# Performance work log

Hardware: AMD Instinct MI355X
Metric: run time of the kernel (lower is better)

The kernel has to match this reference:

```python
import jax, jax.numpy as jnp
import numpy as np

B, T, C = 2, 2048, 1024
H, D = 16, 64
EPS = 1e-6


def _layernorm(x, gamma, beta):
    # Faithful to the torch module: uses unbiased std (Bessel) and divides by (std + eps).
    mean = x.mean(-1, keepdims=True)
    std = jnp.sqrt(jnp.sum((x - mean) ** 2, axis=-1, keepdims=True) / (x.shape[-1] - 1))
    return gamma * (x - mean) / (std + EPS) + beta


def setup_inputs() -> dict:
    key = jax.random.key(0)
    ks = jax.random.split(key, 9)
    s = lambda fan_in: 1.0 / np.sqrt(fan_in)
    return {
        "x": jax.random.normal(ks[0], (B, T, C), dtype=jnp.float32),
        "qkv_w": jax.random.uniform(ks[1], (3 * C, C), jnp.float32, -s(C), s(C)),
        "proj_w": jax.random.uniform(ks[2], (C, C), jnp.float32, -s(C), s(C)),
        "proj_b": jax.random.uniform(ks[3], (C,), jnp.float32, -s(C), s(C)),
        "l1_w": jax.random.uniform(ks[4], (4 * C, C), jnp.float32, -s(C), s(C)),
        "l1_b": jax.random.uniform(ks[5], (4 * C,), jnp.float32, -s(C), s(C)),
        "l3_w": jax.random.uniform(ks[6], (C, 4 * C), jnp.float32, -s(4 * C), s(4 * C)),
        "l3_b": jax.random.uniform(ks[7], (C,), jnp.float32, -s(4 * C), s(4 * C)),
        "ln1_g": jnp.ones((C,), jnp.float32),
        "ln1_b": jnp.zeros((C,), jnp.float32),
        "ln2_g": jnp.ones((C,), jnp.float32),
        "ln2_b": jnp.zeros((C,), jnp.float32),
    }


def _attention(x, qkv_w, proj_w, proj_b):
    Bx, Tx, Cx = x.shape
    qkv = x @ qkv_w.T                      # [B,T,3C]
    q, k, v = jnp.split(qkv, 3, axis=-1)
    q = q.reshape(Bx, Tx, H, D)
    k = k.reshape(Bx, Tx, H, D)
    v = v.reshape(Bx, Tx, H, D)
    scores = jnp.einsum("bthd,bshd->bhts", q, k) * (D ** -0.5)  # [B,H,T,T]
    causal = jnp.tril(jnp.ones((Tx, Tx), dtype=bool))
    scores = jnp.where(causal, scores, -jnp.inf)
    attn = jax.nn.softmax(scores, axis=-1)
    out = jnp.einsum("bhts,bshd->bthd", attn, v).reshape(Bx, Tx, Cx)
    return out @ proj_w.T + proj_b


def _mlp(x, l1_w, l1_b, l3_w, l3_b):
    h = jax.nn.relu(x @ l1_w.T + l1_b)     # [B,T,4C]
    return h @ l3_w.T + l3_b


def reference(x, qkv_w, proj_w, proj_b, l1_w, l1_b, l3_w, l3_b, ln1_g, ln1_b, ln2_g, ln2_b):
    # Dropout is identity in eval mode.
    x1 = x + _attention(_layernorm(x, ln1_g, ln1_b), qkv_w, proj_w, proj_b)
    x2 = x1 + _mlp(_layernorm(x1, ln2_g, ln2_b), l1_w, l1_b, l3_w, l3_b)
    return x2
```

## Files before the change

### kernel.cpp

```cpp
#include <hip/hip_runtime.h>

typedef unsigned short u16;
typedef short short8 __attribute__((ext_vector_type(8)));
typedef float floatx4 __attribute__((ext_vector_type(4)));

#define TT 2048
#define CC 1024

__device__ __forceinline__ u16 f2bf(float f) {
  unsigned int u = __float_as_uint(f);
  u += 0x7fffu + ((u >> 16) & 1u);
  return (u16)(u >> 16);
}

__device__ __forceinline__ void glds16(const u16* g, u16* l) {
  __builtin_amdgcn_global_load_lds((const __attribute__((address_space(1))) void*)g,
                                   (__attribute__((address_space(3))) void*)l, 16, 0, 0);
}

__global__ __launch_bounds__(256) void cvt_all_kernel(const float* __restrict__ w0,
                                                      const float* __restrict__ w1,
                                                      const float* __restrict__ w2,
                                                      const float* __restrict__ w3,
                                                      u16* __restrict__ o0,
                                                      u16* __restrict__ o1,
                                                      u16* __restrict__ o2,
                                                      u16* __restrict__ o3) {
  int blk = blockIdx.x;
  const float* in;
  u16* out;
  int base;
  if (blk < 3072)      { in = w0; out = o0; base = 0; }
  else if (blk < 4096) { in = w1; out = o1; base = 3072; }
  else if (blk < 8192) { in = w2; out = o2; base = 4096; }
  else                 { in = w3; out = o3; base = 8192; }
  int i = (blk - base) * 256 + threadIdx.x;
  float4 v = ((const float4*)in)[i];
  ushort4 o;
  o.x = f2bf(v.x); o.y = f2bf(v.y); o.z = f2bf(v.z); o.w = f2bf(v.w);
  ((ushort4*)out)[i] = o;
}

__global__ __launch_bounds__(256) void ln_kernel(const float* __restrict__ x,
                                                 const float* __restrict__ g,
                                                 const float* __restrict__ b,
                                                 u16* __restrict__ out) {
  int row = blockIdx.x;
  int tid = threadIdx.x;
  const float4* xr = (const float4*)(x + (size_t)row * CC);
  float4 v = xr[tid];
  float s = v.x + v.y + v.z + v.w;
  float sq = v.x * v.x + v.y * v.y + v.z * v.z + v.w * v.w;
#pragma unroll
  for (int off = 1; off < 64; off <<= 1) {
    s += __shfl_xor(s, off);
    sq += __shfl_xor(sq, off);
  }
  __shared__ float ss[4], ssq[4];
  int wave = tid >> 6;
  if ((tid & 63) == 0) { ss[wave] = s; ssq[wave] = sq; }
  __syncthreads();
  s = ss[0] + ss[1] + ss[2] + ss[3];
  sq = ssq[0] + ssq[1] + ssq[2] + ssq[3];
  float mean = s * (1.0f / CC);
  float var = (sq - (float)CC * mean * mean) * (1.0f / (CC - 1));
  float inv = 1.0f / (sqrtf(fmaxf(var, 0.0f)) + 1e-6f);
  float4 gv = ((const float4*)g)[tid];
  float4 bv = ((const float4*)b)[tid];
  ushort4 o;
  o.x = f2bf(gv.x * (v.x - mean) * inv + bv.x);
  o.y = f2bf(gv.y * (v.y - mean) * inv + bv.y);
  o.z = f2bf(gv.z * (v.z - mean) * inv + bv.z);
  o.w = f2bf(gv.w * (v.w - mean) * inv + bv.w);
  ((ushort4*)(out + (size_t)row * CC))[tid] = o;
}

template <int BM, int MODE>
__global__ __launch_bounds__(256) void gemm_bt(const u16* __restrict__ A,
                                               const u16* __restrict__ W,
                                               const float* __restrict__ bias,
                                               const float* __restrict__ resid,
                                               float* __restrict__ outf,
                                               u16* __restrict__ outb,
                                               int M, int N, int K) {
  constexpr int MI = BM / 32;
  __shared__ u16 a_lds[BM * 64];
  __shared__ u16 b_lds[128 * 64];
  int tid = threadIdx.x;
  int w = tid >> 6, lane = tid & 63;
  int l15 = lane & 15, quad = lane >> 4;
  int wm = (w >> 1) * (MI * 16), wn = (w & 1) * 64;
  int tm = blockIdx.x * BM, tn = blockIdx.y * 128;
  floatx4 acc[MI][4];
#pragma unroll
  for (int i = 0; i < MI; i++)
#pragma unroll
    for (int j = 0; j < 4; j++) acc[i][j] = (floatx4){0.f, 0.f, 0.f, 0.f};

  int rsub = lane >> 3;
  int cg = (lane & 7) ^ rsub;
  const u16* Ag = A + (size_t)(tm + w * (BM / 4) + rsub) * K + cg * 8;
  const u16* Bg = W + (size_t)(tn + w * 32 + rsub) * K + cg * 8;
  u16* aL = a_lds + w * (BM / 4) * 64;
  u16* bL = b_lds + w * 32 * 64;

  int x = l15 & 7;
  int offA[MI], offB[4];
#pragma unroll
  for (int i = 0; i < MI; i++) offA[i] = (wm + i * 16 + l15) * 64 + ((quad ^ x) * 8);
#pragma unroll
  for (int j = 0; j < 4; j++) offB[j] = (wn + j * 16 + l15) * 64 + ((quad ^ x) * 8);

  for (int k0 = 0; k0 < K; k0 += 64) {
    __syncthreads();
#pragma unroll
    for (int is = 0; is < BM / 32; is++) glds16(Ag + k0 + is * 8 * K, aL + is * 512);
#pragma unroll
    for (int is = 0; is < 4; is++) glds16(Bg + k0 + is * 8 * K, bL + is * 512);
    __syncthreads();
#pragma unroll
    for (int s = 0; s < 2; s++) {
      short8 af[MI], bw[4];
#pragma unroll
      for (int i = 0; i < MI; i++) af[i] = *(const short8*)(a_lds + (offA[i] ^ (s << 5)));
#pragma unroll
      for (int j = 0; j < 4; j++) bw[j] = *(const short8*)(b_lds + (offB[j] ^ (s << 5)));
#pragma unroll
      for (int i = 0; i < MI; i++)
#pragma unroll
        for (int j = 0; j < 4; j++)
          acc[i][j] = __builtin_amdgcn_mfma_f32_16x16x32_bf16(af[i], bw[j], acc[i][j], 0, 0, 0);
    }
  }

#pragma unroll
  for (int i = 0; i < MI; i++) {
    int row0 = tm + wm + i * 16 + quad * 4;
#pragma unroll
    for (int j = 0; j < 4; j++) {
      int col = tn + wn + j * 16 + l15;
      float bb = (MODE != 0) ? bias[col] : 0.0f;
#pragma unroll
      for (int r = 0; r < 4; r++) {
        int row = row0 + r;
        float v = acc[i][j][r];
        if (MODE == 0) {
          if (col < 1024) v *= 0.125f;
          outb[(size_t)row * N + col] = f2bf(v);
        } else if (MODE == 1) {
          outf[(size_t)row * N + col] = v + bb + resid[(size_t)row * N + col];
        } else {
          outb[(size_t)row * N + col] = f2bf(fmaxf(v + bb, 0.0f));
        }
      }
    }
  }
}

__global__ __launch_bounds__(256) void flash_kernel(const u16* __restrict__ qkv,
                                                    u16* __restrict__ attn) {
  int bid = blockIdx.x;
  int qt = 31 - (bid >> 5);
  int bh = bid & 31;
  int b = bh >> 4, h = bh & 15;
  int tid = threadIdx.x, w = tid >> 6, lane = tid & 63;
  int l15 = lane & 15, quad = lane >> 4;

  __shared__ u16 k_lds[64 * 64];
  __shared__ u16 vt_lds[64 * 72];
  __shared__ u16 p_lds[4][16 * 72];

  int qbase = qt * 64 + w * 16;
  const u16* qp = qkv + (size_t)(b * TT + qbase + l15) * 3072 + h * 64;
  short8 qf0 = *(const short8*)(qp + quad * 8);
  short8 qf1 = *(const short8*)(qp + 32 + quad * 8);

  float m_i = -3.0e38f, l_i = 0.0f;
  floatx4 accO[4];
#pragma unroll
  for (int jf = 0; jf < 4; jf++) accO[jf] = (floatx4){0.f, 0.f, 0.f, 0.f};

  int rsub = lane >> 3;
  int cg = (lane & 7) ^ rsub;
  const u16* Kg = qkv + (size_t)(b * TT + w * 16 + rsub) * 3072 + 1024 + h * 64 + cg * 8;
  u16* kL = k_lds + w * 16 * 64;
  int sV = tid & 63, d0v = (tid >> 6) * 16;
  const u16* Vg = qkv + (size_t)(b * TT + sV) * 3072 + 2048 + h * 64 + d0v;

  int x = l15 & 7;
  int kOff[4], vOff[4];
#pragma unroll
  for (int i = 0; i < 4; i++) kOff[i] = (i * 16 + l15) * 64 + ((quad ^ x) * 8);
#pragma unroll
  for (int jf = 0; jf < 4; jf++) vOff[jf] = (jf * 16 + l15) * 72 + quad * 8;
  int pRd = l15 * 72 + quad * 8;

  int kt_end = qt + 1;
  for (int kt = 0; kt < kt_end; kt++) {
    int s0 = kt * 64;
    size_t soff = (size_t)s0 * 3072;
    uint4 v0 = *(const uint4*)(Vg + soff);
    uint4 v1 = *(const uint4*)(Vg + soff + 8);
    __syncthreads();
#pragma unroll
    for (int is = 0; is < 2; is++) glds16(Kg + soff + (size_t)is * 8 * 3072, kL + is * 512);
    {
      u16 tmp[16];
      *(uint4*)tmp = v0;
      *(uint4*)(tmp + 8) = v1;
#pragma unroll
      for (int j = 0; j < 16; j++) vt_lds[(d0v + j) * 72 + sV] = tmp[j];
    }
    __syncthreads();

    floatx4 st[4];
#pragma unroll
    for (int i = 0; i < 4; i++) st[i] = (floatx4){0.f, 0.f, 0.f, 0.f};
#pragma unroll
    for (int i = 0; i < 4; i++) {
      short8 kf0 = *(const short8*)(k_lds + kOff[i]);
      short8 kf1 = *(const short8*)(k_lds + (kOff[i] ^ 32));
      st[i] = __builtin_amdgcn_mfma_f32_16x16x32_bf16(kf0, qf0, st[i], 0, 0, 0);
      st[i] = __builtin_amdgcn_mfma_f32_16x16x32_bf16(kf1, qf1, st[i], 0, 0, 0);
    }

    if (s0 + 63 > qbase + 15) {
      int mg = qbase + l15;
#pragma unroll
      for (int i = 0; i < 4; i++)
#pragma unroll
        for (int r = 0; r < 4; r++) {
          int s = s0 + i * 16 + quad * 4 + r;
          if (s > mg) st[i][r] = -3.0e38f;
        }
    }

    float mx = st[0][0];
#pragma unroll
    for (int i = 0; i < 4; i++)
#pragma unroll
      for (int r = 0; r < 4; r++) mx = fmaxf(mx, st[i][r]);
    mx = fmaxf(mx, __shfl_xor(mx, 16));
    mx = fmaxf(mx, __shfl_xor(mx, 32));
    float mnew = fmaxf(m_i, mx);
    float alpha = __expf(m_i - mnew);
    float ts = 0.0f;
#pragma unroll
    for (int i = 0; i < 4; i++)
#pragma unroll
      for (int r = 0; r < 4; r++) {
        float p = __expf(st[i][r] - mnew);
        st[i][r] = p;
        ts += p;
      }
    ts += __shfl_xor(ts, 16);
    ts += __shfl_xor(ts, 32);
    l_i = l_i * alpha + ts;
    m_i = mnew;

    float aR[4];
#pragma unroll
    for (int r = 0; r < 4; r++) aR[r] = __shfl(alpha, quad * 4 + r);
#pragma unroll
    for (int jf = 0; jf < 4; jf++)
#pragma unroll
      for (int r = 0; r < 4; r++) accO[jf][r] *= aR[r];

#pragma unroll
    for (int i = 0; i < 4; i++) {
      unsigned int lo = (unsigned int)f2bf(st[i][0]) | ((unsigned int)f2bf(st[i][1]) << 16);
      unsigned int hi = (unsigned int)f2bf(st[i][2]) | ((unsigned int)f2bf(st[i][3]) << 16);
      uint2 pk = {lo, hi};
      *(uint2*)(p_lds[w] + l15 * 72 + i * 16 + quad * 4) = pk;
    }

    short8 pf0 = *(const short8*)(p_lds[w] + pRd);
    short8 pf1 = *(const short8*)(p_lds[w] + pRd + 32);
#pragma unroll
    for (int jf = 0; jf < 4; jf++) {
      short8 vf0 = *(const short8*)(vt_lds + vOff[jf]);
      short8 vf1 = *(const short8*)(vt_lds + vOff[jf] + 32);
      accO[jf] = __builtin_amdgcn_mfma_f32_16x16x32_bf16(pf0, vf0, accO[jf], 0, 0, 0);
      accO[jf] = __builtin_amdgcn_mfma_f32_16x16x32_bf16(pf1, vf1, accO[jf], 0, 0, 0);
    }
  }

  float invl = 1.0f / l_i;
  float iR[4];
#pragma unroll
  for (int r = 0; r < 4; r++) iR[r] = __shfl(invl, quad * 4 + r);
  int orow = b * TT + qbase + quad * 4;
#pragma unroll
  for (int r = 0; r < 4; r++) {
    u16* op = attn + (size_t)(orow + r) * CC + h * 64 + l15;
#pragma unroll
    for (int jf = 0; jf < 4; jf++) op[jf * 16] = f2bf(accO[jf][r] * iR[r]);
  }
}

extern "C" void kernel_launch(void* const* d_in, const int* in_sizes, int n_in,
                              void* d_out, int out_size, void* d_ws, size_t ws_size,
                              hipStream_t stream) {
  const float* x      = (const float*)d_in[0];
  const float* qkv_w  = (const float*)d_in[1];
  const float* proj_w = (const float*)d_in[2];
  const float* proj_b = (const float*)d_in[3];
  const float* l1_w   = (const float*)d_in[4];
  const float* l1_b   = (const float*)d_in[5];
  const float* l3_w   = (const float*)d_in[6];
  const float* l3_b   = (const float*)d_in[7];
  const float* ln1_g  = (const float*)d_in[8];
  const float* ln1_b  = (const float*)d_in[9];
  const float* ln2_g  = (const float*)d_in[10];
  const float* ln2_b  = (const float*)d_in[11];
  float* out = (float*)d_out;
  char* ws = (char*)d_ws;

  u16* w_qkv  = (u16*)(ws + 0);
  u16* w_proj = (u16*)(ws + 6291456);
  u16* w_l1   = (u16*)(ws + 8388608);
  u16* w_l3   = (u16*)(ws + 16777216);
  u16* lnb    = (u16*)(ws + 25165824);
  u16* qkvb   = (u16*)(ws + 33554432);
  u16* attnb  = (u16*)(ws + 58720256);
  float* x1   = (float*)(ws + 67108864);
  u16* hb     = (u16*)(ws + 83886080);

  cvt_all_kernel<<<12288, 256, 0, stream>>>(qkv_w, proj_w, l1_w, l3_w,
                                            w_qkv, w_proj, w_l1, w_l3);

  ln_kernel<<<4096, 256, 0, stream>>>(x, ln1_g, ln1_b, lnb);
  gemm_bt<128, 0><<<dim3(32, 24), 256, 0, stream>>>(lnb, w_qkv, nullptr, nullptr, nullptr,
                                                    qkvb, 4096, 3072, 1024);
  flash_kernel<<<1024, 256, 0, stream>>>(qkvb, attnb);
  gemm_bt<64, 1><<<dim3(64, 8), 256, 0, stream>>>(attnb, w_proj, proj_b, x, x1, nullptr,
                                                  4096, 1024, 1024);
  ln_kernel<<<4096, 256, 0, stream>>>(x1, ln2_g, ln2_b, lnb);
  gemm_bt<128, 2><<<dim3(32, 32), 256, 0, stream>>>(lnb, w_l1, l1_b, nullptr, nullptr, hb,
                                                    4096, 4096, 1024);
  gemm_bt<64, 1><<<dim3(64, 8), 256, 0, stream>>>(hb, w_l3, l3_b, x1, out, nullptr,
                                                  4096, 1024, 4096);
}
```

Baseline: 350.2 us.

## Split-K the final MLP GEMM and widen flash-attention key tiles to 128

The last MLP GEMM (K=4096) is split into two K halves launched along grid z. Each half writes fp32 partials into a reused workspace region, and a separate reduce kernel adds the partials, bias and residual. This doubles the block count for a GEMM that previously had only 512 blocks. Separately, the flash kernel now processes 128 keys per iteration instead of 64, halving loop overhead and barriers at the cost of more LDS and registers. The split-K path adds extra fp32 global traffic.

```diff
diff --git a/kernel.cpp b/kernel.cpp
--- a/kernel.cpp
+++ b/kernel.cpp
@@ -82,7 +82,7 @@
                                                const float* __restrict__ resid,
                                                float* __restrict__ outf,
                                                u16* __restrict__ outb,
-                                               int M, int N, int K) {
+                                               int M, int N, int K, int lda) {
   constexpr int MI = BM / 32;
   __shared__ u16 a_lds[BM * 64];
   __shared__ u16 b_lds[128 * 64];
@@ -91,6 +91,7 @@
   int l15 = lane & 15, quad = lane >> 4;
   int wm = (w >> 1) * (MI * 16), wn = (w & 1) * 64;
   int tm = blockIdx.x * BM, tn = blockIdx.y * 128;
+  size_t koff = (size_t)blockIdx.z * K;
   floatx4 acc[MI][4];
 #pragma unroll
   for (int i = 0; i < MI; i++)
@@ -99,8 +100,8 @@
 
   int rsub = lane >> 3;
   int cg = (lane & 7) ^ rsub;
-  const u16* Ag = A + (size_t)(tm + w * (BM / 4) + rsub) * K + cg * 8;
-  const u16* Bg = W + (size_t)(tn + w * 32 + rsub) * K + cg * 8;
+  const u16* Ag = A + (size_t)(tm + w * (BM / 4) + rsub) * lda + koff + cg * 8;
+  const u16* Bg = W + (size_t)(tn + w * 32 + rsub) * lda + koff + cg * 8;
   u16* aL = a_lds + w * (BM / 4) * 64;
   u16* bL = b_lds + w * 32 * 64;
 
@@ -114,9 +115,9 @@
   for (int k0 = 0; k0 < K; k0 += 64) {
     __syncthreads();
 #pragma unroll
-    for (int is = 0; is < BM / 32; is++) glds16(Ag + k0 + is * 8 * K, aL + is * 512);
-#pragma unroll
-    for (int is = 0; is < 4; is++) glds16(Bg + k0 + is * 8 * K, bL + is * 512);
+    for (int is = 0; is < BM / 32; is++) glds16(Ag + k0 + (size_t)is * 8 * lda, aL + is * 512);
+#pragma unroll
+    for (int is = 0; is < 4; is++) glds16(Bg + k0 + (size_t)is * 8 * lda, bL + is * 512);
     __syncthreads();
 #pragma unroll
     for (int s = 0; s < 2; s++) {
@@ -133,13 +134,14 @@
     }
   }
 
+  float* po = (MODE == 3) ? outf + (size_t)blockIdx.z * M * N : outf;
 #pragma unroll
   for (int i = 0; i < MI; i++) {
     int row0 = tm + wm + i * 16 + quad * 4;
 #pragma unroll
     for (int j = 0; j < 4; j++) {
       int col = tn + wn + j * 16 + l15;
-      float bb = (MODE != 0) ? bias[col] : 0.0f;
+      float bb = (MODE == 1 || MODE == 2) ? bias[col] : 0.0f;
 #pragma unroll
       for (int r = 0; r < 4; r++) {
         int row = row0 + r;
@@ -149,12 +151,31 @@
           outb[(size_t)row * N + col] = f2bf(v);
         } else if (MODE == 1) {
           outf[(size_t)row * N + col] = v + bb + resid[(size_t)row * N + col];
+        } else if (MODE == 2) {
+          outb[(size_t)row * N + col] = f2bf(fmaxf(v + bb, 0.0f));
         } else {
-          outb[(size_t)row * N + col] = f2bf(fmaxf(v + bb, 0.0f));
+          po[(size_t)row * N + col] = v;
         }
       }
     }
   }
+}
+
+__global__ __launch_bounds__(256) void reduce2_kernel(const float* __restrict__ p,
+                                                      const float* __restrict__ bias,
+                                                      const float* __restrict__ resid,
+                                                      float* __restrict__ out) {
+  int i = blockIdx.x * 256 + threadIdx.x;
+  float4 a = ((const float4*)p)[i];
+  float4 b = ((const float4*)p)[i + 1048576];
+  float4 r = ((const float4*)resid)[i];
+  float4 bb = ((const float4*)bias)[i & 255];
+  float4 o;
+  o.x = a.x + b.x + r.x + bb.x;
+  o.y = a.y + b.y + r.y + bb.y;
+  o.z = a.z + b.z + r.z + bb.z;
+  o.w = a.w + b.w + r.w + bb.w;
+  ((float4*)out)[i] = o;
 }
 
 __global__ __launch_bounds__(256) void flash_kernel(const u16* __restrict__ qkv,
@@ -166,9 +187,9 @@
   int tid = threadIdx.x, w = tid >> 6, lane = tid & 63;
   int l15 = lane & 15, quad = lane >> 4;
 
-  __shared__ u16 k_lds[64 * 64];
-  __shared__ u16 vt_lds[64 * 72];
-  __shared__ u16 p_lds[4][16 * 72];
+  __shared__ u16 k_lds[128 * 64];
+  __shared__ u16 vt_lds[64 * 136];
+  __shared__ u16 p_lds[4][16 * 136];
 
   int qbase = qt * 64 + w * 16;
   const u16* qp = qkv + (size_t)(b * TT + qbase + l15) * 3072 + h * 64;
@@ -182,52 +203,54 @@
 
   int rsub = lane >> 3;
   int cg = (lane & 7) ^ rsub;
-  const u16* Kg = qkv + (size_t)(b * TT + w * 16 + rsub) * 3072 + 1024 + h * 64 + cg * 8;
-  u16* kL = k_lds + w * 16 * 64;
-  int sV = tid & 63, d0v = (tid >> 6) * 16;
+  const u16* Kg = qkv + (size_t)(b * TT + w * 32 + rsub) * 3072 + 1024 + h * 64 + cg * 8;
+  u16* kL = k_lds + w * 32 * 64;
+  int sV = tid & 127, d0v = (tid >> 7) * 32;
   const u16* Vg = qkv + (size_t)(b * TT + sV) * 3072 + 2048 + h * 64 + d0v;
 
   int x = l15 & 7;
-  int kOff[4], vOff[4];
-#pragma unroll
-  for (int i = 0; i < 4; i++) kOff[i] = (i * 16 + l15) * 64 + ((quad ^ x) * 8);
-#pragma unroll
-  for (int jf = 0; jf < 4; jf++) vOff[jf] = (jf * 16 + l15) * 72 + quad * 8;
-  int pRd = l15 * 72 + quad * 8;
-
-  int kt_end = qt + 1;
-  for (int kt = 0; kt < kt_end; kt++) {
-    int s0 = kt * 64;
+  int kOff[8];
+#pragma unroll
+  for (int i = 0; i < 8; i++) kOff[i] = (i * 16 + l15) * 64 + ((quad ^ x) * 8);
+  int pRd = l15 * 136 + quad * 8;
+
+  int nt = (qt + 2) >> 1;
+  for (int kt = 0; kt < nt; kt++) {
+    int s0 = kt * 128;
     size_t soff = (size_t)s0 * 3072;
     uint4 v0 = *(const uint4*)(Vg + soff);
     uint4 v1 = *(const uint4*)(Vg + soff + 8);
+    uint4 v2 = *(const uint4*)(Vg + soff + 16);
+    uint4 v3 = *(const uint4*)(Vg + soff + 24);
     __syncthreads();
 #pragma unroll
-    for (int is = 0; is < 2; is++) glds16(Kg + soff + (size_t)is * 8 * 3072, kL + is * 512);
+    for (int is = 0; is < 4; is++) glds16(Kg + soff + (size_t)is * 8 * 3072, kL + is * 512);
     {
-      u16 tmp[16];
+      u16 tmp[32];
       *(uint4*)tmp = v0;
       *(uint4*)(tmp + 8) = v1;
-#pragma unroll
-      for (int j = 0; j < 16; j++) vt_lds[(d0v + j) * 72 + sV] = tmp[j];
+      *(uint4*)(tmp + 16) = v2;
+      *(uint4*)(tmp + 24) = v3;
+#pragma unroll
+      for (int j = 0; j < 32; j++) vt_lds[(d0v + j) * 136 + sV] = tmp[j];
     }
     __syncthreads();
 
-    floatx4 st[4];
-#pragma unroll
-    for (int i = 0; i < 4; i++) st[i] = (floatx4){0.f, 0.f, 0.f, 0.f};
-#pragma unroll
-    for (int i = 0; i < 4; i++) {
+    floatx4 st[8];
+#pragma unroll
+    for (int i = 0; i < 8; i++) st[i] = (floatx4){0.f, 0.f, 0.f, 0.f};
+#pragma unroll
+    for (int i = 0; i < 8; i++) {
       short8 kf0 = *(const short8*)(k_lds + kOff[i]);
       short8 kf1 = *(const short8*)(k_lds + (kOff[i] ^ 32));
       st[i] = __builtin_amdgcn_mfma_f32_16x16x32_bf16(kf0, qf0, st[i], 0, 0, 0);
       st[i] = __builtin_amdgcn_mfma_f32_16x16x32_bf16(kf1, qf1, st[i], 0, 0, 0);
     }
 
-    if (s0 + 63 > qbase + 15) {
+    if (s0 + 127 > qbase) {
       int mg = qbase + l15;
 #pragma unroll
-      for (int i = 0; i < 4; i++)
+      for (int i = 0; i < 8; i++)
 #pragma unroll
         for (int r = 0; r < 4; r++) {
           int s = s0 + i * 16 + quad * 4 + r;
@@ -237,7 +260,7 @@
 
     float mx = st[0][0];
 #pragma unroll
-    for (int i = 0; i < 4; i++)
+    for (int i = 0; i < 8; i++)
 #pragma unroll
       for (int r = 0; r < 4; r++) mx = fmaxf(mx, st[i][r]);
     mx = fmaxf(mx, __shfl_xor(mx, 16));
@@ -246,7 +269,7 @@
     float alpha = __expf(m_i - mnew);
     float ts = 0.0f;
 #pragma unroll
-    for (int i = 0; i < 4; i++)
+    for (int i = 0; i < 8; i++)
 #pragma unroll
       for (int r = 0; r < 4; r++) {
         float p = __expf(st[i][r] - mnew);
@@ -267,21 +290,24 @@
       for (int r = 0; r < 4; r++) accO[jf][r] *= aR[r];
 
 #pragma unroll
-    for (int i = 0; i < 4; i++) {
+    for (int i = 0; i < 8; i++) {
       unsigned int lo = (unsigned int)f2bf(st[i][0]) | ((unsigned int)f2bf(st[i][1]) << 16);
       unsigned int hi = (unsigned int)f2bf(st[i][2]) | ((unsigned int)f2bf(st[i][3]) << 16);
       uint2 pk = {lo, hi};
-      *(uint2*)(p_lds[w] + l15 * 72 + i * 16 + quad * 4) = pk;
-    }
-
-    short8 pf0 = *(const short8*)(p_lds[w] + pRd);
-    short8 pf1 = *(const short8*)(p_lds[w] + pRd + 32);
+      *(uint2*)(p_lds[w] + l15 * 136 + i * 16 + quad * 4) = pk;
+    }
+
+    short8 pf[4];
+#pragma unroll
+    for (int c = 0; c < 4; c++) pf[c] = *(const short8*)(p_lds[w] + pRd + c * 32);
 #pragma unroll
     for (int jf = 0; jf < 4; jf++) {
-      short8 vf0 = *(const short8*)(vt_lds + vOff[jf]);
-      short8 vf1 = *(const short8*)(vt_lds + vOff[jf] + 32);
-      accO[jf] = __builtin_amdgcn_mfma_f32_16x16x32_bf16(pf0, vf0, accO[jf], 0, 0, 0);
-      accO[jf] = __builtin_amdgcn_mfma_f32_16x16x32_bf16(pf1, vf1, accO[jf], 0, 0, 0);
+      int vOff = (jf * 16 + l15) * 136 + quad * 8;
+#pragma unroll
+      for (int c = 0; c < 4; c++) {
+        short8 vf = *(const short8*)(vt_lds + vOff + c * 32);
+        accO[jf] = __builtin_amdgcn_mfma_f32_16x16x32_bf16(pf[c], vf, accO[jf], 0, 0, 0);
+      }
     }
   }
 
@@ -325,19 +351,21 @@
   u16* attnb  = (u16*)(ws + 58720256);
   float* x1   = (float*)(ws + 67108864);
   u16* hb     = (u16*)(ws + 83886080);
+  float* l3p  = (float*)(ws + 33554432);
 
   cvt_all_kernel<<<12288, 256, 0, stream>>>(qkv_w, proj_w, l1_w, l3_w,
                                             w_qkv, w_proj, w_l1, w_l3);
 
   ln_kernel<<<4096, 256, 0, stream>>>(x, ln1_g, ln1_b, lnb);
   gemm_bt<128, 0><<<dim3(32, 24), 256, 0, stream>>>(lnb, w_qkv, nullptr, nullptr, nullptr,
-                                                    qkvb, 4096, 3072, 1024);
+                                                    qkvb, 4096, 3072, 1024, 1024);
   flash_kernel<<<1024, 256, 0, stream>>>(qkvb, attnb);
   gemm_bt<64, 1><<<dim3(64, 8), 256, 0, stream>>>(attnb, w_proj, proj_b, x, x1, nullptr,
-                                                  4096, 1024, 1024);
+                                                  4096, 1024, 1024, 1024);
   ln_kernel<<<4096, 256, 0, stream>>>(x1, ln2_g, ln2_b, lnb);
   gemm_bt<128, 2><<<dim3(32, 32), 256, 0, stream>>>(lnb, w_l1, l1_b, nullptr, nullptr, hb,
-                                                    4096, 4096, 1024);
-  gemm_bt<64, 1><<<dim3(64, 8), 256, 0, stream>>>(hb, w_l3, l3_b, x1, out, nullptr,
-                                                  4096, 1024, 4096);
-}
+                                                    4096, 4096, 1024, 1024);
+  gemm_bt<64, 3><<<dim3(64, 8, 2), 256, 0, stream>>>(hb, w_l3, nullptr, nullptr, l3p,
+                                                     nullptr, 4096, 1024, 2048, 4096);
+  reduce2_kernel<<<4096, 256, 0, stream>>>(l3p, l3_b, x1, out);
+}
```

New measurement: 328.8 us. 6.1% less time.
